# Optimization experiments

Measured on AMD Instinct MI355X. Metric: run time of the kernel, lower is better.

The kernel has to match this reference:

```python
import jax, jax.numpy as jnp
import numpy as np

K = 5          # number of neighbors (topk k=5+1, drop self)
EPS = 1e-05    # hparams['epsilon'] for gentropy term


def setup_inputs() -> dict:
    key = jax.random.key(0)
    k1, k2, k3, k4, k5 = jax.random.split(key, 5)
    B, D, C, N = 256, 256, 64, 200000
    features = jax.random.normal(k1, (B, D), dtype=jnp.float32)
    W = jax.random.normal(k2, (D, C), dtype=jnp.float32) * 0.05
    b = jnp.zeros((C,), dtype=jnp.float32)
    fea_bank = jax.random.normal(k3, (N, D), dtype=jnp.float32)
    # score bank holds softmax outputs -> make rows valid probability distributions
    score_bank = jax.nn.softmax(jax.random.normal(k4, (N, C), dtype=jnp.float32), axis=-1)
    trg_idx = jax.random.randint(k5, (B,), 0, N, dtype=jnp.int64)
    return {"features": features, "W": W, "b": b,
            "fea_bank": fea_bank, "score_bank": score_bank, "trg_idx": trg_idx}


def reference(features, W, b, fea_bank, score_bank, trg_idx):
    sg = jax.lax.stop_gradient
    B = features.shape[0]
    C = W.shape[1]

    logits = features @ W + b                       # classifier(features)
    softmax_out = jax.nn.softmax(logits, axis=-1)   # [B, C] (differentiable)

    # --- everything bank-related is under torch.no_grad in the original ---
    nrm = jnp.maximum(jnp.linalg.norm(features, axis=1, keepdims=True), 1e-12)
    f_norm = sg(features / nrm)                     # F.normalize(features)
    fb = sg(fea_bank.at[trg_idx].set(f_norm))        # fea_bank[trg_idx] = f_norm
    sb = sg(score_bank.at[trg_idx].set(sg(softmax_out)))

    dist = f_norm @ fb.T                             # [B, N]
    _, idx_near = jax.lax.top_k(dist, K + 1)
    idx_near = idx_near[:, 1:]                       # [B, K] drop self

    score_near = sb[idx_near]                        # [B, K, C]
    fea_near = fb[idx_near]                          # [B, K, D]

    dist2 = jnp.einsum('bkd,nd->bkn', fea_near, fb)  # [B, K, N]
    _, idx_nn = jax.lax.top_k(dist2, K + 1)
    idx_nn = idx_nn[:, :, 1:]                        # [B, K, K]

    match = (idx_nn == trg_idx[:, None, None]).sum(-1).astype(jnp.float32)  # [B, K]
    weight = jnp.where(match > 0.0, match, jnp.float32(0.1))                # [B, K]
    weight_kk = jnp.full((B, K * K), 0.1, dtype=jnp.float32)  # fill_(0.1) overwrites

    score_near_kk = sb[idx_nn].reshape(B, K * K, C)  # [B, K*K, C]
    # --- end no_grad region ---

    # F.kl_div(input, target, reduction='none') = target * (log(target) - input)
    # (original passes probabilities, not log-probs, as input -- kept faithfully)
    kl_kk = score_near_kk * (jnp.log(score_near_kk) - softmax_out[:, None, :])
    loss = jnp.mean((kl_kk.sum(-1) * weight_kk).sum(1))

    kl_n = score_near * (jnp.log(score_near) - softmax_out[:, None, :])
    loss = loss + jnp.mean((kl_n.sum(-1) * weight).sum(1))

    msoftmax = softmax_out.mean(axis=0)
    gentropy = jnp.sum(msoftmax * jnp.log(msoftmax + EPS))
    loss = loss + gentropy
    return loss
```

## Files before the change

kernel.cpp:

```cpp
#include <hip/hip_runtime.h>
#include <hip/hip_bf16.h>
#include <math.h>

#define B_SZ   256
#define D_DIM  256
#define C_DIM  64
#define N_CAND 200000
#define K_TOP  5
#define CH32   32
#define CH32_SH 8192
#define QTILE_SH 16384
#define NCH32  (N_CAND / CH32)
#define CMSTR  6256
#define NCHJ1  16
#define NCHJ2  32
#define S1     ((NCH32 + NCHJ1 - 1) / NCHJ1)
#define S2     ((NCH32 + NCHJ2 - 1) / NCHJ2)
#define MAXC   192

typedef short bf16x8 __attribute__((ext_vector_type(8)));
typedef float f32x16 __attribute__((ext_vector_type(16)));
typedef unsigned short u16x8 __attribute__((ext_vector_type(8)));

__device__ __forceinline__ bool better(float v1, int i1, float v2, int i2) {
    return (v1 > v2) || (v1 == v2 && i1 < i2);
}

__device__ __forceinline__ void insert6f(float* lv, int* li, float v, int idx) {
    if (better(v, idx, lv[5], li[5])) {
        lv[5] = v; li[5] = idx;
        #pragma unroll
        for (int k = 5; k > 0; --k) {
            if (better(lv[k], li[k], lv[k - 1], li[k - 1])) {
                float tv = lv[k]; lv[k] = lv[k - 1]; lv[k - 1] = tv;
                int   ti = li[k]; li[k] = li[k - 1]; li[k - 1] = ti;
            }
        }
    }
}

__device__ __forceinline__ void merge6(const float* av, const int* ai,
                                       const float* bv, const int* bi,
                                       float* ov, int* oi) {
    int ia = 0, ib = 0;
    #pragma unroll
    for (int k = 0; k < 6; ++k) {
        bool ta;
        if (ia >= 6)      ta = false;
        else if (ib >= 6) ta = true;
        else              ta = better(av[ia], ai[ia], bv[ib], bi[ib]);
        if (ta) { ov[k] = av[ia]; oi[k] = ai[ia]; ++ia; }
        else    { ov[k] = bv[ib]; oi[k] = bi[ib]; ++ib; }
    }
}

__device__ __forceinline__ unsigned short bf16rne(float x) {
    unsigned int u = __float_as_uint(x);
    unsigned int r = u + 0x7fffu + ((u >> 16) & 1u);
    return (unsigned short)(r >> 16);
}

__device__ __forceinline__ float bf16f(unsigned short h) {
    return __uint_as_float(((unsigned)h) << 16);
}

__device__ __forceinline__ u16x8 pack8(float4 a, float4 b) {
    u16x8 h;
    h[0] = bf16rne(a.x); h[1] = bf16rne(a.y); h[2] = bf16rne(a.z); h[3] = bf16rne(a.w);
    h[4] = bf16rne(b.x); h[5] = bf16rne(b.y); h[6] = bf16rne(b.z); h[7] = bf16rne(b.w);
    return h;
}

__global__ void k_init(int* pos_of, float* accp) {
    int i = blockIdx.x * 256 + threadIdx.x;
    if (i < N_CAND) pos_of[i] = -1;
    if (i == 0) accp[0] = 0.f;
}

__global__ void k_scatter(const int* __restrict__ trg, int* __restrict__ pos_of) {
    int j = threadIdx.x;
    atomicMax(&pos_of[trg[j]], j);
}

__global__ __launch_bounds__(256) void k_prep(const float* __restrict__ features,
                                              const float* __restrict__ W,
                                              const float* __restrict__ bias,
                                              float* __restrict__ f_norm,
                                              float* __restrict__ softm) {
    int b = blockIdx.x, t = threadIdx.x;
    __shared__ float row[256];
    __shared__ float red[256];
    float x = features[b * D_DIM + t];
    row[t] = x; red[t] = x * x;
    __syncthreads();
    for (int s = 128; s > 0; s >>= 1) {
        if (t < s) red[t] += red[t + s];
        __syncthreads();
    }
    float nrm = fmaxf(sqrtf(red[0]), 1e-12f);
    f_norm[b * D_DIM + t] = x / nrm;
    if (t < C_DIM) {
        float acc = bias[t];
        for (int d = 0; d < D_DIM; ++d) acc = fmaf(row[d], W[d * C_DIM + t], acc);
        float mx = acc;
        for (int off = 32; off > 0; off >>= 1) mx = fmaxf(mx, __shfl_xor(mx, off, 64));
        float e = expf(acc - mx);
        float ssum = e;
        for (int off = 32; off > 0; off >>= 1) ssum += __shfl_xor(ssum, off, 64);
        softm[b * C_DIM + t] = e / ssum;
    }
}

__global__ __launch_bounds__(256) void k_convert(const float* __restrict__ fea_bank,
                                                 const float* __restrict__ f_norm,
                                                 const int* __restrict__ pos_of,
                                                 short* __restrict__ bank) {
    int cc = blockIdx.x, t = threadIdx.x;
    int r = t >> 2, q4 = t & 3;
    int n = cc * 64 + r;
    int p = pos_of[n];
    const float* src = (p >= 0) ? (f_norm + (size_t)p * D_DIM)
                                : (fea_bank + (size_t)n * D_DIM);
    short* dst = bank + (size_t)(cc * 2 + (r >> 5)) * CH32_SH;
    int rl = r & 31;
    #pragma unroll
    for (int i = 0; i < 8; ++i) {
        int kk = q4 * 64 + i * 8;
        float4 a = *(const float4*)(src + kk);
        float4 b = *(const float4*)(src + kk + 4);
        int e = ((kk >> 4) * 64) + (((kk >> 3) & 1) * 32) + rl;
        *(u16x8*)(dst + (size_t)e * 8) = pack8(a, b);
    }
}

__global__ __launch_bounds__(256) void k_permq(const float* __restrict__ rows,
                                               const float* __restrict__ fea_bank,
                                               const int* __restrict__ idx,
                                               const int* __restrict__ pos_of,
                                               short* __restrict__ dst,
                                               unsigned short* __restrict__ qplain) {
    int tile = blockIdx.x, t = threadIdx.x;
    int r = t >> 2, q4 = t & 3;
    const float* src;
    if (idx) {
        int n = idx[tile * 64 + r];
        int p = pos_of[n];
        src = (p >= 0) ? (rows + (size_t)p * D_DIM) : (fea_bank + (size_t)n * D_DIM);
    } else {
        src = rows + (size_t)(tile * 64 + r) * D_DIM;
    }
    short* d = dst + (size_t)tile * QTILE_SH;
    unsigned short* qp = qplain + (size_t)(tile * 64 + r) * D_DIM;
    #pragma unroll
    for (int i = 0; i < 8; ++i) {
        int kk = q4 * 64 + i * 8;
        float4 a = *(const float4*)(src + kk);
        float4 b = *(const float4*)(src + kk + 4);
        u16x8 h = pack8(a, b);
        int e = ((kk >> 4) * 128) + ((r >> 5) * 64) + (((kk >> 3) & 1) * 32) + (r & 31);
        *(u16x8*)(d + (size_t)e * 8) = h;
        *(u16x8*)(qp + kk) = h;
    }
}

__global__ __launch_bounds__(256, 2) void dist_max(const short* __restrict__ qbf,
                                                   const short* __restrict__ bank,
                                                   unsigned short* __restrict__ cmax,
                                                   int nqt, int swz,
                                                   int S, int nchj) {
    __shared__ __align__(16) short sbuf[2 * CH32_SH];
    __shared__ unsigned short cmaxbuf[32 * 256];

    int slab, qt;
    if (swz) {
        int bid = blockIdx.x;
        int xcd = bid & 7;
        int rem = bid >> 3;
        qt = rem % nqt;
        slab = (rem / nqt) * 8 + xcd;
        if (slab >= S) return;
    } else {
        slab = blockIdx.x;
        qt = blockIdx.y;
    }
    const int cfirst = slab * nchj;
    int nch = NCH32 - cfirst; if (nch > nchj) nch = nchj;

    const int t   = threadIdx.x;
    const int w   = t >> 6;
    const int l   = t & 63;
    const int khv = l >> 5;
    const int col = l & 31;

    const short* qtile = qbf + (size_t)(qt * 4 + w) * QTILE_SH;
    bf16x8 bfr0[16], bfr1[16];
    #pragma unroll
    for (int ks = 0; ks < 16; ++ks) {
        bfr0[ks] = *(const bf16x8*)(qtile + (size_t)(ks * 128      + l) * 8);
        bfr1[ks] = *(const bf16x8*)(qtile + (size_t)(ks * 128 + 64 + l) * 8);
    }
    #pragma unroll
    for (int ks = 0; ks < 16; ++ks)
        asm volatile("" : "+v"(bfr0[ks]), "+v"(bfr1[ks]));

    const short* sbase = bank + (size_t)cfirst * CH32_SH;

    #pragma unroll
    for (int i = 0; i < 4; ++i) {
        const short* gp = sbase + (size_t)(i * 256 + t) * 8;
        short* lp = sbuf + (size_t)(i * 256 + w * 64) * 8;
        __builtin_amdgcn_global_load_lds(
            (const __attribute__((address_space(1))) void*)gp,
            (__attribute__((address_space(3))) void*)lp, 16, 0, 0);
    }

    for (int ch = 0; ch < nch; ++ch) {
        const int cur = ch & 1;
        if (ch + 1 < nch) {
            const short* g = sbase + (size_t)(ch + 1) * CH32_SH;
            short* lbase = sbuf + (size_t)(cur ^ 1) * CH32_SH;
            #pragma unroll
            for (int i = 0; i < 4; ++i) {
                const short* gp = g + (size_t)(i * 256 + t) * 8;
                short* lp = lbase + (size_t)(i * 256 + w * 64) * 8;
                __builtin_amdgcn_global_load_lds(
                    (const __attribute__((address_space(1))) void*)gp,
                    (__attribute__((address_space(3))) void*)lp, 16, 0, 0);
            }
            asm volatile("s_waitcnt vmcnt(4)" ::: "memory");
        } else {
            asm volatile("s_waitcnt vmcnt(0)" ::: "memory");
        }
        __builtin_amdgcn_s_barrier();
        __builtin_amdgcn_sched_barrier(0);

        const short* cb = sbuf + (size_t)cur * CH32_SH;

        f32x16 a0 = {}, a1 = {};
        #pragma unroll
        for (int ks = 0; ks < 16; ++ks) {
            bf16x8 fa = *(const bf16x8*)(cb + (size_t)(ks * 64 + l) * 8);
            a0 = __builtin_amdgcn_mfma_f32_32x32x16_bf16(fa, bfr0[ks], a0, 0, 0, 0);
            a1 = __builtin_amdgcn_mfma_f32_32x32x16_bf16(fa, bfr1[ks], a1, 0, 0, 0);
        }

        float m0 = a0[0], m1 = a1[0];
        #pragma unroll
        for (int r = 1; r < 16; ++r) { m0 = fmaxf(m0, a0[r]); m1 = fmaxf(m1, a1[r]); }
        m0 = fmaxf(m0, __shfl_xor(m0, 32, 64));
        m1 = fmaxf(m1, __shfl_xor(m1, 32, 64));
        if (khv == 0) {
            cmaxbuf[ch * 256 + w * 64 + col]      = bf16rne(m0);
            cmaxbuf[ch * 256 + w * 64 + 32 + col] = bf16rne(m1);
        }

        __builtin_amdgcn_sched_barrier(0);
        __builtin_amdgcn_s_barrier();
    }

    __syncthreads();
    {
        size_t gbase = (size_t)(qt * 256 + t) * CMSTR + cfirst;
        int c0 = 0;
        for (; c0 + 8 <= nch; c0 += 8) {
            u16x8 h;
            #pragma unroll
            for (int i = 0; i < 8; ++i) h[i] = cmaxbuf[(c0 + i) * 256 + t];
            *(u16x8*)(cmax + gbase + c0) = h;
        }
        for (; c0 < nch; ++c0) cmax[gbase + c0] = cmaxbuf[c0 * 256 + t];
    }
}

__global__ __launch_bounds__(256) void k_select(const unsigned short* __restrict__ cmax,
                                                const unsigned short* __restrict__ qplain,
                                                const short* __restrict__ bank,
                                                int* __restrict__ out_idx) {
    int q = blockIdx.x, t = threadIdx.x;
    __shared__ float sv[256][6];
    __shared__ int   si[256][6];
    __shared__ float qrow[256];
    __shared__ int cnt;
    __shared__ int list[MAXC];

    const unsigned short* row = cmax + (size_t)q * CMSTR;

    float lv[6]; int li[6];
    #pragma unroll
    for (int k = 0; k < 6; ++k) { lv[k] = -3.4e38f; li[k] = 0x7fffffff; }
    for (int c = t; c < NCH32; c += 256) insert6f(lv, li, bf16f(row[c]), c);
    #pragma unroll
    for (int k = 0; k < 6; ++k) { sv[t][k] = lv[k]; si[t][k] = li[k]; }
    if (t == 0) cnt = 0;
    __syncthreads();
    for (int w = 128; w >= 1; w >>= 1) {
        if (t < w) {
            float ov[6]; int oi[6];
            merge6(sv[t], si[t], sv[t + w], si[t + w], ov, oi);
            #pragma unroll
            for (int k = 0; k < 6; ++k) { sv[t][k] = ov[k]; si[t][k] = oi[k]; }
        }
        __syncthreads();
    }
    float tauM = sv[0][5] - 6e-3f;
    __syncthreads();

    for (int c = t; c < NCH32; c += 256) {
        if (bf16f(row[c]) >= tauM) {
            int k = atomicAdd(&cnt, 1);
            if (k < MAXC) list[k] = c;
        }
    }
    qrow[t] = bf16f(qplain[(size_t)q * D_DIM + t]);
    __syncthreads();
    int nc = cnt < MAXC ? cnt : MAXC;

    float bv[6]; int bi[6];
    #pragma unroll
    for (int k = 0; k < 6; ++k) { bv[k] = -3.4e38f; bi[k] = 0x7fffffff; }
    const int cand = t >> 3, j = t & 7;
    for (int ci = 0; ci < nc; ++ci) {
        int c = list[ci];
        const short* cb = bank + (size_t)c * CH32_SH;
        u16x8 h0 = *(const u16x8*)(cb + (size_t)(128 * j +  0 + cand) * 8);
        u16x8 h1 = *(const u16x8*)(cb + (size_t)(128 * j + 32 + cand) * 8);
        u16x8 h2 = *(const u16x8*)(cb + (size_t)(128 * j + 64 + cand) * 8);
        u16x8 h3 = *(const u16x8*)(cb + (size_t)(128 * j + 96 + cand) * 8);
        int d0 = j * 32;
        float acc = 0.f;
        #pragma unroll
        for (int d = 0; d < 8; ++d) {
            acc = fmaf(bf16f(h0[d]), qrow[d0 + d], acc);
            acc = fmaf(bf16f(h1[d]), qrow[d0 + 8 + d], acc);
            acc = fmaf(bf16f(h2[d]), qrow[d0 + 16 + d], acc);
            acc = fmaf(bf16f(h3[d]), qrow[d0 + 24 + d], acc);
        }
        acc += __shfl_down(acc, 4, 8);
        acc += __shfl_down(acc, 2, 8);
        acc += __shfl_down(acc, 1, 8);
        if (j == 0) insert6f(bv, bi, acc, c * CH32 + cand);
    }

    #pragma unroll
    for (int k = 0; k < 6; ++k) { sv[t][k] = bv[k]; si[t][k] = bi[k]; }
    __syncthreads();
    for (int w = 128; w >= 1; w >>= 1) {
        if (t < w) {
            float ov[6]; int oi[6];
            merge6(sv[t], si[t], sv[t + w], si[t + w], ov, oi);
            #pragma unroll
            for (int k = 0; k < 6; ++k) { sv[t][k] = ov[k]; si[t][k] = oi[k]; }
        }
        __syncthreads();
    }
    if (t == 0) {
        for (int k = 1; k < 6; ++k) out_idx[q * K_TOP + k - 1] = si[0][k];
    }
}

__global__ void k_loss(const float* __restrict__ softm, const float* __restrict__ score_bank,
                       const int* __restrict__ pos_of, const int* __restrict__ idx_near,
                       const int* __restrict__ idx_nn, const int* __restrict__ trg,
                       float* accp) {
    int b = blockIdx.x, c = threadIdx.x;
    float p_bc = softm[b * C_DIM + c];
    float part = 0.f;
    for (int k = 0; k < K_TOP; ++k) {
        for (int j = 0; j < K_TOP; ++j) {
            int n = idx_nn[(b * K_TOP + k) * K_TOP + j];
            int p = pos_of[n];
            const float* srow = (p >= 0) ? (softm + (size_t)p * C_DIM)
                                         : (score_bank + (size_t)n * C_DIM);
            float s = srow[c];
            float v = s * (logf(s) - p_bc);
            for (int off = 32; off > 0; off >>= 1) v += __shfl_down(v, off, 64);
            if (c == 0) part += 0.1f * v;
        }
    }
    for (int k = 0; k < K_TOP; ++k) {
        int n = idx_near[b * K_TOP + k];
        int p = pos_of[n];
        const float* srow = (p >= 0) ? (softm + (size_t)p * C_DIM)
                                     : (score_bank + (size_t)n * C_DIM);
        float s = srow[c];
        float v = s * (logf(s) - p_bc);
        for (int off = 32; off > 0; off >>= 1) v += __shfl_down(v, off, 64);
        if (c == 0) {
            int m = 0;
            for (int j = 0; j < K_TOP; ++j)
                m += (idx_nn[(b * K_TOP + k) * K_TOP + j] == trg[b]) ? 1 : 0;
            float w = (m > 0) ? (float)m : 0.1f;
            part += w * v;
        }
    }
    if (c == 0) atomicAdd(accp, part * (1.0f / (float)B_SZ));
}

__global__ void k_final(const float* __restrict__ softm, const float* __restrict__ accp,
                        float* __restrict__ out) {
    int c = threadIdx.x;
    float m = 0.f;
    for (int b = 0; b < B_SZ; ++b) m += softm[b * C_DIM + c];
    m *= (1.0f / (float)B_SZ);
    float g = m * logf(m + 1e-5f);
    for (int off = 32; off > 0; off >>= 1) g += __shfl_down(g, off, 64);
    if (c == 0) out[0] = accp[0] + g;
}

extern "C" void kernel_launch(void* const* d_in, const int* in_sizes, int n_in,
                              void* d_out, int out_size, void* d_ws, size_t ws_size,
                              hipStream_t stream) {
    const float* features   = (const float*)d_in[0];
    const float* W          = (const float*)d_in[1];
    const float* bias       = (const float*)d_in[2];
    const float* fea_bank   = (const float*)d_in[3];
    const float* score_bank = (const float*)d_in[4];
    const int*   trg        = (const int*)d_in[5];
    float* out = (float*)d_out;

    char* ws = (char*)d_ws;
    size_t off = 0;
    auto alloc = [&](size_t bytes) -> void* {
        void* p = ws + off;
        off = (off + bytes + 255) & ~(size_t)255;
        return p;
    };
    short* bankbf   = (short*)alloc((size_t)NCH32 * CH32_SH * 2);
    short* q1bf     = (short*)alloc((size_t)(B_SZ / 64) * QTILE_SH * 2);
    short* q2bf     = (short*)alloc((size_t)(B_SZ * K_TOP / 64) * QTILE_SH * 2);
    unsigned short* qplain1 = (unsigned short*)alloc((size_t)B_SZ * D_DIM * 2);
    unsigned short* qplain2 = (unsigned short*)alloc((size_t)B_SZ * K_TOP * D_DIM * 2);
    float* f_norm   = (float*)alloc((size_t)B_SZ * D_DIM * 4);
    float* softm    = (float*)alloc((size_t)B_SZ * C_DIM * 4);
    int*   pos_of   = (int*)alloc((size_t)N_CAND * 4);
    float* accp     = (float*)alloc(4);
    int*   idx_near = (int*)alloc((size_t)B_SZ * K_TOP * 4);
    int*   idx_nn   = (int*)alloc((size_t)B_SZ * K_TOP * K_TOP * 4);
    unsigned short* cmax1 = (unsigned short*)alloc((size_t)B_SZ * CMSTR * 2);
    unsigned short* cmax2 = (unsigned short*)alloc((size_t)B_SZ * K_TOP * CMSTR * 2);

    k_init<<<dim3((N_CAND + 255) / 256), dim3(256), 0, stream>>>(pos_of, accp);
    k_scatter<<<dim3(1), dim3(256), 0, stream>>>(trg, pos_of);
    k_prep<<<dim3(B_SZ), dim3(256), 0, stream>>>(features, W, bias, f_norm, softm);

    k_convert<<<dim3(NCH32 / 2), dim3(256), 0, stream>>>(fea_bank, f_norm, pos_of, bankbf);
    k_permq<<<dim3(B_SZ / 64), dim3(256), 0, stream>>>(
        f_norm, fea_bank, nullptr, pos_of, q1bf, qplain1);

    dist_max<<<dim3(S1, 1), dim3(256), 0, stream>>>(
        q1bf, bankbf, cmax1, 1, 0, S1, NCHJ1);
    k_select<<<dim3(B_SZ), dim3(256), 0, stream>>>(cmax1, qplain1, bankbf, idx_near);

    k_permq<<<dim3(B_SZ * K_TOP / 64), dim3(256), 0, stream>>>(
        f_norm, fea_bank, idx_near, pos_of, q2bf, qplain2);

    {
        int nqt = (B_SZ * K_TOP) / 256;
        int nsg = (S2 + 7) / 8;
        dist_max<<<dim3(nsg * 8 * nqt), dim3(256), 0, stream>>>(
            q2bf, bankbf, cmax2, nqt, 1, S2, NCHJ2);
    }
    k_select<<<dim3(B_SZ * K_TOP), dim3(256), 0, stream>>>(cmax2, qplain2, bankbf, idx_nn);

    k_loss<<<dim3(B_SZ), dim3(64), 0, stream>>>(softm, score_bank, pos_of, idx_near, idx_nn, trg, accp);
    k_final<<<dim3(1), dim3(64), 0, stream>>>(softm, accp, out);
}
```

Measured before the change: 358.6 us.

## Deepen dist_max LDS pipeline to four buffers and vectorize select scans

The dist_max kernel moves from double to quadruple LDS buffering, prefetching three chunks ahead. It drops the trailing barrier, issues the next prefetch after compute, and raises wave priority around the MFMA loop, all to hide global-load latency better. The convert and permute kernels reorder their per-thread column offsets so that neighbouring lanes read contiguous memory. k_select now reads cmax rows as 8-wide vectors with a per-group max prefilter, which needs dist_max to fill padding entries with a bf16 sentinel. This doubles LDS use per block, which could reduce occupancy, and it relies on the padding writes to keep the scan correct.

```diff
diff --git a/kernel.cpp b/kernel.cpp
--- a/kernel.cpp
+++ b/kernel.cpp
@@ -125,7 +125,7 @@
     int rl = r & 31;
     #pragma unroll
     for (int i = 0; i < 8; ++i) {
-        int kk = q4 * 64 + i * 8;
+        int kk = i * 32 + q4 * 8;
         float4 a = *(const float4*)(src + kk);
         float4 b = *(const float4*)(src + kk + 4);
         int e = ((kk >> 4) * 64) + (((kk >> 3) & 1) * 32) + rl;
@@ -153,7 +153,7 @@
     unsigned short* qp = qplain + (size_t)(tile * 64 + r) * D_DIM;
     #pragma unroll
     for (int i = 0; i < 8; ++i) {
-        int kk = q4 * 64 + i * 8;
+        int kk = i * 32 + q4 * 8;
         float4 a = *(const float4*)(src + kk);
         float4 b = *(const float4*)(src + kk + 4);
         u16x8 h = pack8(a, b);
@@ -168,7 +168,7 @@
                                                    unsigned short* __restrict__ cmax,
                                                    int nqt, int swz,
                                                    int S, int nchj) {
-    __shared__ __align__(16) short sbuf[2 * CH32_SH];
+    __shared__ __align__(16) short sbuf[4 * CH32_SH];
     __shared__ unsigned short cmaxbuf[32 * 256];
 
     int slab, qt;
@@ -206,19 +206,52 @@
     const short* sbase = bank + (size_t)cfirst * CH32_SH;
 
     #pragma unroll
-    for (int i = 0; i < 4; ++i) {
-        const short* gp = sbase + (size_t)(i * 256 + t) * 8;
-        short* lp = sbuf + (size_t)(i * 256 + w * 64) * 8;
-        __builtin_amdgcn_global_load_lds(
-            (const __attribute__((address_space(1))) void*)gp,
-            (__attribute__((address_space(3))) void*)lp, 16, 0, 0);
+    for (int c = 0; c < 3; ++c) {
+        const short* g = sbase + (size_t)c * CH32_SH;
+        short* lbase = sbuf + (size_t)c * CH32_SH;
+        #pragma unroll
+        for (int i = 0; i < 4; ++i) {
+            const short* gp = g + (size_t)(i * 256 + t) * 8;
+            short* lp = lbase + (size_t)(i * 256 + w * 64) * 8;
+            __builtin_amdgcn_global_load_lds(
+                (const __attribute__((address_space(1))) void*)gp,
+                (__attribute__((address_space(3))) void*)lp, 16, 0, 0);
+        }
     }
 
     for (int ch = 0; ch < nch; ++ch) {
-        const int cur = ch & 1;
-        if (ch + 1 < nch) {
-            const short* g = sbase + (size_t)(ch + 1) * CH32_SH;
-            short* lbase = sbuf + (size_t)(cur ^ 1) * CH32_SH;
+        int ahead = nch - 1 - ch;
+        if (ahead >= 2)      asm volatile("s_waitcnt vmcnt(8)" ::: "memory");
+        else if (ahead == 1) asm volatile("s_waitcnt vmcnt(4)" ::: "memory");
+        else                 asm volatile("s_waitcnt vmcnt(0)" ::: "memory");
+        __builtin_amdgcn_s_barrier();
+        __builtin_amdgcn_sched_barrier(0);
+
+        const short* cb = sbuf + (size_t)(ch & 3) * CH32_SH;
+
+        f32x16 a0 = {}, a1 = {};
+        __builtin_amdgcn_s_setprio(1);
+        #pragma unroll
+        for (int ks = 0; ks < 16; ++ks) {
+            bf16x8 fa = *(const bf16x8*)(cb + (size_t)(ks * 64 + l) * 8);
+            a0 = __builtin_amdgcn_mfma_f32_32x32x16_bf16(fa, bfr0[ks], a0, 0, 0, 0);
+            a1 = __builtin_amdgcn_mfma_f32_32x32x16_bf16(fa, bfr1[ks], a1, 0, 0, 0);
+        }
+        __builtin_amdgcn_s_setprio(0);
+
+        float m0 = a0[0], m1 = a1[0];
+        #pragma unroll
+        for (int r = 1; r < 16; ++r) { m0 = fmaxf(m0, a0[r]); m1 = fmaxf(m1, a1[r]); }
+        m0 = fmaxf(m0, __shfl_xor(m0, 32, 64));
+        m1 = fmaxf(m1, __shfl_xor(m1, 32, 64));
+        if (khv == 0) {
+            cmaxbuf[ch * 256 + w * 64 + col]      = bf16rne(m0);
+            cmaxbuf[ch * 256 + w * 64 + 32 + col] = bf16rne(m1);
+        }
+
+        if (ch + 3 < nch) {
+            const short* g = sbase + (size_t)(ch + 3) * CH32_SH;
+            short* lbase = sbuf + (size_t)((ch + 3) & 3) * CH32_SH;
             #pragma unroll
             for (int i = 0; i < 4; ++i) {
                 const short* gp = g + (size_t)(i * 256 + t) * 8;
@@ -227,35 +260,7 @@
                     (const __attribute__((address_space(1))) void*)gp,
                     (__attribute__((address_space(3))) void*)lp, 16, 0, 0);
             }
-            asm volatile("s_waitcnt vmcnt(4)" ::: "memory");
-        } else {
-            asm volatile("s_waitcnt vmcnt(0)" ::: "memory");
-        }
-        __builtin_amdgcn_s_barrier();
-        __builtin_amdgcn_sched_barrier(0);
-
-        const short* cb = sbuf + (size_t)cur * CH32_SH;
-
-        f32x16 a0 = {}, a1 = {};
-        #pragma unroll
-        for (int ks = 0; ks < 16; ++ks) {
-            bf16x8 fa = *(const bf16x8*)(cb + (size_t)(ks * 64 + l) * 8);
-            a0 = __builtin_amdgcn_mfma_f32_32x32x16_bf16(fa, bfr0[ks], a0, 0, 0, 0);
-            a1 = __builtin_amdgcn_mfma_f32_32x32x16_bf16(fa, bfr1[ks], a1, 0, 0, 0);
-        }
-
-        float m0 = a0[0], m1 = a1[0];
-        #pragma unroll
-        for (int r = 1; r < 16; ++r) { m0 = fmaxf(m0, a0[r]); m1 = fmaxf(m1, a1[r]); }
-        m0 = fmaxf(m0, __shfl_xor(m0, 32, 64));
-        m1 = fmaxf(m1, __shfl_xor(m1, 32, 64));
-        if (khv == 0) {
-            cmaxbuf[ch * 256 + w * 64 + col]      = bf16rne(m0);
-            cmaxbuf[ch * 256 + w * 64 + 32 + col] = bf16rne(m1);
-        }
-
-        __builtin_amdgcn_sched_barrier(0);
-        __builtin_amdgcn_s_barrier();
+        }
     }
 
     __syncthreads();
@@ -269,6 +274,8 @@
             *(u16x8*)(cmax + gbase + c0) = h;
         }
         for (; c0 < nch; ++c0) cmax[gbase + c0] = cmaxbuf[c0 * 256 + t];
+        int cend = CMSTR - cfirst; if (cend > nchj) cend = nchj;
+        for (int cp = nch; cp < cend; ++cp) cmax[gbase + cp] = 0xFF7F;
     }
 }
 
@@ -288,7 +295,19 @@
     float lv[6]; int li[6];
     #pragma unroll
     for (int k = 0; k < 6; ++k) { lv[k] = -3.4e38f; li[k] = 0x7fffffff; }
-    for (int c = t; c < NCH32; c += 256) insert6f(lv, li, bf16f(row[c]), c);
+    for (int c0 = t * 8; c0 < CMSTR; c0 += 2048) {
+        u16x8 h = *(const u16x8*)(row + c0);
+        float m8 = bf16f(h[0]);
+        #pragma unroll
+        for (int i = 1; i < 8; ++i) m8 = fmaxf(m8, bf16f(h[i]));
+        if (better(m8, c0, lv[5], li[5])) {
+            #pragma unroll
+            for (int i = 0; i < 8; ++i) {
+                int c = c0 + i;
+                if (c < NCH32) insert6f(lv, li, bf16f(h[i]), c);
+            }
+        }
+    }
     #pragma unroll
     for (int k = 0; k < 6; ++k) { sv[t][k] = lv[k]; si[t][k] = li[k]; }
     if (t == 0) cnt = 0;
@@ -305,10 +324,20 @@
     float tauM = sv[0][5] - 6e-3f;
     __syncthreads();
 
-    for (int c = t; c < NCH32; c += 256) {
-        if (bf16f(row[c]) >= tauM) {
-            int k = atomicAdd(&cnt, 1);
-            if (k < MAXC) list[k] = c;
+    for (int c0 = t * 8; c0 < CMSTR; c0 += 2048) {
+        u16x8 h = *(const u16x8*)(row + c0);
+        float m8 = bf16f(h[0]);
+        #pragma unroll
+        for (int i = 1; i < 8; ++i) m8 = fmaxf(m8, bf16f(h[i]));
+        if (m8 >= tauM) {
+            #pragma unroll
+            for (int i = 0; i < 8; ++i) {
+                int c = c0 + i;
+                if (c < NCH32 && bf16f(h[i]) >= tauM) {
+                    int k = atomicAdd(&cnt, 1);
+                    if (k < MAXC) list[k] = c;
+                }
+            }
         }
     }
     qrow[t] = bf16f(qplain[(size_t)q * D_DIM + t]);
```

After: 317.2 us. 1.13x faster.
